# Performance work log

Hardware: AMD Instinct MI355X
Metric: run time of the kernel (lower is better)

Reference implementation:

```python
import jax, jax.numpy as jnp
import numpy as np

B, T, D, H, O = 64, 512, 512, 1024, 512

def _xavier(key, shape):
    fan_out, fan_in = shape
    limit = np.sqrt(6.0 / (fan_in + fan_out))
    return jax.random.uniform(key, shape, jnp.float32, -limit, limit)

def setup_inputs() -> dict:
    key = jax.random.key(0)
    k_in, k_wx, k_wh, k_wo = jax.random.split(key, 4)
    inputs = jax.random.normal(k_in, (B, T, D), dtype=jnp.float32)
    Wx = _xavier(k_wx, (3 * H, D))   # x2h weight (n*H, D)
    bx = jnp.zeros((3 * H,), jnp.float32)
    Wh = _xavier(k_wh, (3 * H, H))   # h2h weight (n*H, H)
    bh = jnp.zeros((3 * H,), jnp.float32)
    Wo = _xavier(k_wo, (O, H))       # output head
    bo = jnp.zeros((O,), jnp.float32)
    return {"inputs": inputs, "Wx": Wx, "bx": bx, "Wh": Wh, "bh": bh, "Wo": Wo, "bo": bo}

def _gru(inputs, Wx, bx, Wh, bh):
    # precompute input projection for all timesteps: (B, T, 3H)
    x_all = jnp.einsum('btd,gd->btg', inputs, Wx) + bx

    def step(h, x_t):
        # h: (B, H); x_t: (B, 3H)
        h_proj = h @ Wh.T + bh                  # (B, 3H)
        x_r, x_u, x_n = jnp.split(x_t, 3, axis=-1)
        h_r, h_u, h_n = jnp.split(h_proj, 3, axis=-1)
        reset = jax.nn.sigmoid(x_r + h_r)
        upd = jax.nn.sigmoid(x_u + h_u)
        new = jnp.tanh(x_n + reset * h_n)       # activation='tanh'
        hy = upd * h + (1.0 - upd) * new
        return hy, hy

    h0 = jnp.zeros((inputs.shape[0], Wh.shape[1]), inputs.dtype)
    _, hs = jax.lax.scan(step, h0, jnp.swapaxes(x_all, 0, 1))  # hs: (T, B, H)
    return jnp.swapaxes(hs, 0, 1)               # (B, T, H)

def reference(inputs, Wx, bx, Wh, bh, Wo, bo):
    hiddens = _gru(inputs, Wx, bx, Wh, bh)       # (B, T, H)
    out = jnp.einsum('bth,oh->bto', hiddens, Wo) + bo  # (B, T, O)
    return hiddens, out
```

## Files before the change

kernel.cpp:

```cpp
#include <hip/hip_runtime.h>
#include <hip/hip_bf16.h>

typedef __attribute__((ext_vector_type(8))) short short8;
typedef __attribute__((ext_vector_type(4))) float float4v;

__device__ __forceinline__ float bf2f(short b) {
    unsigned u = ((unsigned)(unsigned short)b) << 16;
    union { unsigned u; float f; } c; c.u = u; return c.f;
}
__device__ __forceinline__ short f2bf(float f) {
    union { float f; unsigned u; } c; c.f = f;
    unsigned r = 0x7FFFu + ((c.u >> 16) & 1u);
    return (short)((c.u + r) >> 16);
}
__device__ __forceinline__ float ldf(const void* p, size_t i, bool f32) {
    return f32 ? ((const float*)p)[i] : bf2f(((const short*)p)[i]);
}
__device__ __forceinline__ short8 frag8(const void* p, size_t i, bool f32) {
    short8 r;
    if (f32) {
        const float* q = (const float*)p + i;
#pragma unroll
        for (int j = 0; j < 8; j++) r[j] = f2bf(q[j]);
    } else {
        r = *(const short8*)((const short*)p + i);
    }
    return r;
}

__global__ __launch_bounds__(256) void dpm_spin(const float* __restrict__ seed,
                                               float* __restrict__ sink, int iters)
{
    float a = seed[threadIdx.x & 15];
    float b = seed[(threadIdx.x & 15) + 16];
    a = (a > 2.f || a < -2.f || (a < 0.01f && a > -0.01f)) ? 1.0000001f : a;
    float x = b + 1.f;
    int n = iters * 16;
#pragma unroll 16
    for (int i = 0; i < n; i++) x = __builtin_fmaf(x, a, b);
    if (x == 12345.6789f) sink[(((size_t)blockIdx.x * 256 + threadIdx.x) & 65535)] = x;
}

__global__ void detect_dtype(const unsigned short* __restrict__ in, unsigned* __restrict__ flag)
{
    int t = threadIdx.x;
    int sane = 0;
    for (int i = t; i < 256; i += 64) {
        unsigned e = (in[i] >> 7) & 0xFF;
        sane += (e >= 0x70 && e <= 0x8A) ? 1 : 0;
    }
#pragma unroll
    for (int o = 32; o > 0; o >>= 1) sane += __shfl_down(sane, o);
    if (t == 0) *flag = (sane >= 200) ? 0u : 1u;
}

__global__ void init_scratch(short* __restrict__ hb, unsigned* __restrict__ cnt)
{
    int i = blockIdx.x * 256 + threadIdx.x;
    if (i < 4 * 65536) hb[i] = 0;
    if (i < 512) cnt[i] = 0;
}

__global__ __launch_bounds__(256, 1) void gemm_bt(
    const void* __restrict__ A, const void* __restrict__ B,
    const void* __restrict__ bias, void* __restrict__ outbase, size_t coff,
    const unsigned* __restrict__ flag, int M, int N, int K)
{
    const bool f32 = flag && (flag[0] != 0u);
    __shared__ short Ah[128][72], Bh[128][72];
    __shared__ short Al[128][72], Bl[128][72];
    const int tid  = threadIdx.x;
    const int wid  = tid >> 6;
    const int lane = tid & 63;
    const int ln = lane & 15, q = lane >> 4;
    const int bm = blockIdx.x * 128, bn = blockIdx.y * 128;
    const int wm = (wid & 1) * 64, wn = (wid >> 1) * 64;

    float4v acc[4][4];
#pragma unroll
    for (int i = 0; i < 4; i++)
#pragma unroll
        for (int j = 0; j < 4; j++) acc[i][j] = (float4v){0.f, 0.f, 0.f, 0.f};

    for (int k0 = 0; k0 < K; k0 += 64) {
#pragma unroll
        for (int c = 0; c < 4; c++) {
            int chunk = tid + c * 256;
            int row = chunk >> 3;
            int kq  = (chunk & 7) * 8;
            size_t ga = (size_t)(bm + row) * K + k0 + kq;
            size_t gb = (size_t)(bn + row) * K + k0 + kq;
            if (f32) {
                const float* Af = (const float*)A;
                const float* Bf = (const float*)B;
#pragma unroll
                for (int j = 0; j < 8; j++) {
                    float av = Af[ga + j], bv = Bf[gb + j];
                    short ah = f2bf(av), bh = f2bf(bv);
                    Ah[row][kq + j] = ah; Al[row][kq + j] = f2bf(av - bf2f(ah));
                    Bh[row][kq + j] = bh; Bl[row][kq + j] = f2bf(bv - bf2f(bh));
                }
            } else {
                *(short8*)&Ah[row][kq] = *(const short8*)((const short*)A + ga);
                *(short8*)&Bh[row][kq] = *(const short8*)((const short*)B + gb);
            }
        }
        __syncthreads();
#pragma unroll
        for (int kt = 0; kt < 2; kt++) {
            short8 avh[4], bvh[4];
#pragma unroll
            for (int i = 0; i < 4; i++) avh[i] = *(const short8*)&Ah[wm + i * 16 + ln][kt * 32 + q * 8];
#pragma unroll
            for (int j = 0; j < 4; j++) bvh[j] = *(const short8*)&Bh[wn + j * 16 + ln][kt * 32 + q * 8];
#pragma unroll
            for (int i = 0; i < 4; i++)
#pragma unroll
                for (int j = 0; j < 4; j++)
                    acc[i][j] = __builtin_amdgcn_mfma_f32_16x16x32_bf16(avh[i], bvh[j], acc[i][j], 0, 0, 0);
            if (f32) {
                short8 avl[4], bvl[4];
#pragma unroll
                for (int i = 0; i < 4; i++) avl[i] = *(const short8*)&Al[wm + i * 16 + ln][kt * 32 + q * 8];
#pragma unroll
                for (int j = 0; j < 4; j++) bvl[j] = *(const short8*)&Bl[wn + j * 16 + ln][kt * 32 + q * 8];
#pragma unroll
                for (int i = 0; i < 4; i++)
#pragma unroll
                    for (int j = 0; j < 4; j++) {
                        acc[i][j] = __builtin_amdgcn_mfma_f32_16x16x32_bf16(avh[i], bvl[j], acc[i][j], 0, 0, 0);
                        acc[i][j] = __builtin_amdgcn_mfma_f32_16x16x32_bf16(avl[i], bvh[j], acc[i][j], 0, 0, 0);
                    }
            }
        }
        __syncthreads();
    }
#pragma unroll
    for (int j = 0; j < 4; j++) {
        int col = bn + wn + j * 16 + ln;
        float bvv = ldf(bias, col, f32);
#pragma unroll
        for (int i = 0; i < 4; i++) {
#pragma unroll
            for (int r = 0; r < 4; r++) {
                int row = bm + wm + i * 16 + q * 4 + r;
                size_t idx = coff + (size_t)row * N + col;
                float v = acc[i][j][r] + bvv;
                if (f32) ((float*)outbase)[idx] = v;
                else     ((short*)outbase)[idx] = f2bf(v);
            }
        }
    }
}

#define NWG 256
__global__ __launch_bounds__(192, 1) void gru_rec(
    const void* __restrict__ inputs,
    const void* __restrict__ Wx,
    const void* __restrict__ bx,
    const void* __restrict__ Wh,
    const void* __restrict__ bh,
    short* __restrict__ hb,
    unsigned* __restrict__ cnt,
    const unsigned* __restrict__ flag,
    void* __restrict__ hid)
{
    const bool f32 = flag && (flag[0] != 0u);
    __shared__ short xs[8192];
    __shared__ short hs[2][16384];
    __shared__ float Px[3][16][17];
    __shared__ float Ph[3][16][17];
    __shared__ float hown[16][17];
    __shared__ float bxs[3][16], bhs[3][16];

    const int tid  = threadIdx.x;
    const int w    = blockIdx.x;
    const int gb   = w >> 6;
    const int c    = w & 63;
    const int g    = tid >> 6;
    const int lane = tid & 63;
    const int ln   = lane & 15, q = lane >> 4;

    const size_t whbase = (size_t)(g * 1024 + c * 16 + ln) * 1024;
    short8 wf[32];
#pragma unroll
    for (int kt = 0; kt < 32; kt++) wf[kt] = frag8(Wh, whbase + kt * 32 + q * 8, f32);

    const size_t wxbase = (size_t)(g * 1024 + c * 16 + ln) * 512;
    short8 wxf[16];
#pragma unroll
    for (int kt = 0; kt < 16; kt++) wxf[kt] = frag8(Wx, wxbase + kt * 32 + q * 8, f32);

    for (int e = tid; e < 256; e += 192) hown[e >> 4][e & 15] = 0.f;
    if (tid < 48) {
        int gg = tid >> 4, jj = tid & 15;
        bxs[gg][jj] = ldf(bx, gg * 1024 + c * 16 + jj, f32);
        bhs[gg][jj] = ldf(bh, gg * 1024 + c * 16 + jj, f32);
    }
    __syncthreads();

    for (int t = 0; t < 512; t++) {
        const short* hsrc = hb + (size_t)((t & 1) ? 2 : 0) * 65536 + gb * 16384;
        short*       hdst = hb + (size_t)((t & 1) ? 0 : 2) * 65536 + gb * 16384;

        float4v ax = (float4v){0.f,0.f,0.f,0.f};
        float4v ah = (float4v){0.f,0.f,0.f,0.f};

        unsigned long long rv[11][2];
        auto load_chunk = [&](int pl) {
            const short* src_ = hsrc + pl * 65536;
#pragma unroll
            for (int i = 0; i < 11; i++) { int e = tid + i * 192; if (e < 2048) {
                const unsigned long long* p_ = (const unsigned long long*)(src_ + e * 8);
                rv[i][0] = __hip_atomic_load(p_,     __ATOMIC_RELAXED, __HIP_MEMORY_SCOPE_AGENT);
                rv[i][1] = __hip_atomic_load(p_ + 1, __ATOMIC_RELAXED, __HIP_MEMORY_SCOPE_AGENT);
            } }
        };
        auto write_chunk = [&](int d) {
#pragma unroll
            for (int i = 0; i < 11; i++) { int e = tid + i * 192; if (e < 2048) {
                int kb = e >> 4, r = e & 15;
                union { unsigned long long qq[2]; short8 v; } u_;
                u_.qq[0] = rv[i][0]; u_.qq[1] = rv[i][1];
                *(short8*)((char*)&hs[d][0] + (kb << 8) + ((r ^ (kb & 15)) << 4)) = u_.v;
            } }
        };

#pragma unroll 4
        for (int i = 0; i < 6; i++) { int e = tid + i * 192; if (e < 1024) {
            int kb = e & 63, r = e >> 6;
            size_t gi = (size_t)(gb * 16 + r) * 262144 + (size_t)t * 512 + kb * 8;
            short8 v = frag8(inputs, gi, f32);
            *(short8*)((char*)xs + (kb << 8) + ((r ^ (kb & 15)) << 4)) = v;
        } }
        __syncthreads();

        if (t) {
            if (tid < 64) {
                const unsigned* fp = &cnt[((t - 1) & 1) * 256 + gb * 64 + tid];
                while (__hip_atomic_load(fp, __ATOMIC_RELAXED, __HIP_MEMORY_SCOPE_AGENT) < (unsigned)t)
                    __builtin_amdgcn_s_sleep(2);
            }
            __syncthreads();
        }

        load_chunk(0);
#pragma unroll
        for (int kt = 0; kt < 16; kt++) {
            int kb = kt * 4 + q;
            short8 a = *(const short8*)((const char*)xs + (kb << 8) + ((ln ^ (kb & 15)) << 4));
            ax = __builtin_amdgcn_mfma_f32_16x16x32_bf16(a, wxf[kt], ax, 0, 0, 0);
        }
        write_chunk(0);
        __syncthreads();

        load_chunk(1);
#pragma unroll
        for (int kt = 0; kt < 32; kt++) {
            int kb = kt * 4 + q;
            short8 a = *(const short8*)((const char*)&hs[0][0] + (kb << 8) + ((ln ^ (kb & 15)) << 4));
            ah = __builtin_amdgcn_mfma_f32_16x16x32_bf16(a, wf[kt], ah, 0, 0, 0);
        }
        write_chunk(1);
        __syncthreads();
#pragma unroll
        for (int kt = 0; kt < 32; kt++) {
            int kb = kt * 4 + q;
            short8 a = *(const short8*)((const char*)&hs[1][0] + (kb << 8) + ((ln ^ (kb & 15)) << 4));
            ah = __builtin_amdgcn_mfma_f32_16x16x32_bf16(a, wf[kt], ah, 0, 0, 0);
        }

#pragma unroll
        for (int r = 0; r < 4; r++) {
            Px[g][q * 4 + r][ln] = ax[r];
            Ph[g][q * 4 + r][ln] = ah[r];
        }
        __syncthreads();

        for (int e = tid; e < 256; e += 192) {
            int r = e >> 4, jj = e & 15;
            float xr = Px[0][r][jj] + bxs[0][jj];
            float xu = Px[1][r][jj] + bxs[1][jj];
            float xn = Px[2][r][jj] + bxs[2][jj];
            float pr = Ph[0][r][jj] + bhs[0][jj];
            float pu = Ph[1][r][jj] + bhs[1][jj];
            float pn = Ph[2][r][jj] + bhs[2][jj];
            float rg = 1.f / (1.f + __expf(-(xr + pr)));
            float ug = 1.f / (1.f + __expf(-(xu + pu)));
            float ng = tanhf(xn + rg * pn);
            float hy = ug * hown[r][jj] + (1.f - ug) * ng;
            hown[r][jj] = hy;
            size_t b = (size_t)(gb * 16 + r);
            size_t hidx = (b * 512 + t) * 1024 + c * 16 + jj;
            if (f32) ((float*)hid)[hidx] = hy;
            else     ((short*)hid)[hidx] = f2bf(hy);
        }
        __syncthreads();

        if (tid < 64) {
            int r = tid & 15, kbl = (tid >> 4) & 1, pl = (tid >> 5) & 1;
            union { unsigned long long qq[2]; short8 v; } u;
#pragma unroll
            for (int j = 0; j < 8; j++) {
                float hy = hown[r][kbl * 8 + j];
                short hh = f2bf(hy);
                u.v[j] = pl ? f2bf(hy - bf2f(hh)) : hh;
            }
            unsigned long long* dp = (unsigned long long*)
                (hdst + (size_t)pl * 65536 + (size_t)(2 * c + kbl) * 128 + r * 8);
            __hip_atomic_store(dp,     u.qq[0], __ATOMIC_RELAXED, __HIP_MEMORY_SCOPE_AGENT);
            __hip_atomic_store(dp + 1, u.qq[1], __ATOMIC_RELAXED, __HIP_MEMORY_SCOPE_AGENT);
        }
        asm volatile("s_waitcnt vmcnt(0)" ::: "memory");
        __syncthreads();

        if (tid == 0)
            __hip_atomic_store(&cnt[(t & 1) * 256 + gb * 64 + c], (unsigned)(t + 1),
                               __ATOMIC_RELAXED, __HIP_MEMORY_SCOPE_AGENT);
    }
}

extern "C" void kernel_launch(void* const* d_in, const int* in_sizes, int n_in,
                              void* d_out, int out_size, void* d_ws, size_t ws_size,
                              hipStream_t stream)
{
    const void* inputs = d_in[0];
    const void* Wx     = d_in[1];
    const void* bx     = d_in[2];
    const void* Wh     = d_in[3];
    const void* bh     = d_in[4];
    const void* Wo     = d_in[5];
    const void* bo     = d_in[6];

    const size_t HID_ELEMS = (size_t)64 * 512 * 1024;

    short* hb; unsigned* cnt; unsigned* flag;
    const bool use_ws = (d_ws != nullptr) && (ws_size >= (size_t)(4096 + 4 * 65536 * 2));
    if (use_ws) {
        cnt  = (unsigned*)d_ws;
        flag = cnt + 512;
        hb   = (short*)((char*)d_ws + 4096);
    } else {
        short* outh = (short*)d_out + HID_ELEMS;
        hb   = outh;
        cnt  = (unsigned*)(outh + 4 * 65536);
        flag = nullptr;
    }

    if (use_ws) detect_dtype<<<1, 64, 0, stream>>>((const unsigned short*)inputs, flag);
    init_scratch<<<1024, 256, 0, stream>>>(hb, cnt);

    gru_rec<<<NWG, 192, 0, stream>>>(inputs, Wx, bx, Wh, bh, hb, cnt, flag, d_out);

    dpm_spin<<<2048, 256, 0, stream>>>((const float*)Wx, (float*)hb, 7032);

    gemm_bt<<<dim3(256, 4), 256, 0, stream>>>(d_out, Wo, bo, d_out, HID_ELEMS, flag, 32768, 512, 1024);
}
```

Baseline: 5.791 ms.

## Prefetch next-step inputs, merge hidden-state plane loads, drop spin kernel

Removes the dpm_spin busy-loop kernel that ran between the recurrence and the output GEMM. Inside the recurrent loop, the next timestep's input fragments are prefetched into registers while the current step computes, and both bf16 planes of the hidden state are loaded in one batch. The flag wait now comes before a single barrier, one trailing barrier is dropped, and f32 fragment loads use vector loads. The cost is more register pressure from the prefetch buffers, which may reduce occupancy.

```diff
diff --git a/kernel.cpp b/kernel.cpp
--- a/kernel.cpp
+++ b/kernel.cpp
@@ -20,25 +20,14 @@
     short8 r;
     if (f32) {
         const float* q = (const float*)p + i;
-#pragma unroll
-        for (int j = 0; j < 8; j++) r[j] = f2bf(q[j]);
+        float4v a = *(const float4v*)q;
+        float4v b = *(const float4v*)(q + 4);
+#pragma unroll
+        for (int j = 0; j < 4; j++) { r[j] = f2bf(a[j]); r[4 + j] = f2bf(b[j]); }
     } else {
         r = *(const short8*)((const short*)p + i);
     }
     return r;
-}
-
-__global__ __launch_bounds__(256) void dpm_spin(const float* __restrict__ seed,
-                                               float* __restrict__ sink, int iters)
-{
-    float a = seed[threadIdx.x & 15];
-    float b = seed[(threadIdx.x & 15) + 16];
-    a = (a > 2.f || a < -2.f || (a < 0.01f && a > -0.01f)) ? 1.0000001f : a;
-    float x = b + 1.f;
-    int n = iters * 16;
-#pragma unroll 16
-    for (int i = 0; i < n; i++) x = __builtin_fmaf(x, a, b);
-    if (x == 12345.6789f) sink[(((size_t)blockIdx.x * 256 + threadIdx.x) & 65535)] = x;
 }
 
 __global__ void detect_dtype(const unsigned short* __restrict__ in, unsigned* __restrict__ flag)
@@ -199,6 +188,13 @@
     }
     __syncthreads();
 
+    short8 xreg[6];
+#pragma unroll
+    for (int i = 0; i < 6; i++) { int e = tid + i * 192; if (e < 1024) {
+        int kb = e & 63, r = e >> 6;
+        xreg[i] = frag8(inputs, (size_t)(gb * 16 + r) * 262144 + kb * 8, f32);
+    } }
+
     for (int t = 0; t < 512; t++) {
         const short* hsrc = hb + (size_t)((t & 1) ? 2 : 0) * 65536 + gb * 16384;
         short*       hdst = hb + (size_t)((t & 1) ? 0 : 2) * 65536 + gb * 16384;
@@ -206,69 +202,61 @@
         float4v ax = (float4v){0.f,0.f,0.f,0.f};
         float4v ah = (float4v){0.f,0.f,0.f,0.f};
 
-        unsigned long long rv[11][2];
-        auto load_chunk = [&](int pl) {
-            const short* src_ = hsrc + pl * 65536;
-#pragma unroll
-            for (int i = 0; i < 11; i++) { int e = tid + i * 192; if (e < 2048) {
-                const unsigned long long* p_ = (const unsigned long long*)(src_ + e * 8);
-                rv[i][0] = __hip_atomic_load(p_,     __ATOMIC_RELAXED, __HIP_MEMORY_SCOPE_AGENT);
-                rv[i][1] = __hip_atomic_load(p_ + 1, __ATOMIC_RELAXED, __HIP_MEMORY_SCOPE_AGENT);
-            } }
-        };
-        auto write_chunk = [&](int d) {
-#pragma unroll
-            for (int i = 0; i < 11; i++) { int e = tid + i * 192; if (e < 2048) {
-                int kb = e >> 4, r = e & 15;
-                union { unsigned long long qq[2]; short8 v; } u_;
-                u_.qq[0] = rv[i][0]; u_.qq[1] = rv[i][1];
-                *(short8*)((char*)&hs[d][0] + (kb << 8) + ((r ^ (kb & 15)) << 4)) = u_.v;
-            } }
-        };
-
-#pragma unroll 4
+#pragma unroll
         for (int i = 0; i < 6; i++) { int e = tid + i * 192; if (e < 1024) {
             int kb = e & 63, r = e >> 6;
-            size_t gi = (size_t)(gb * 16 + r) * 262144 + (size_t)t * 512 + kb * 8;
-            short8 v = frag8(inputs, gi, f32);
-            *(short8*)((char*)xs + (kb << 8) + ((r ^ (kb & 15)) << 4)) = v;
+            *(short8*)((char*)xs + (kb << 8) + ((r ^ (kb & 15)) << 4)) = xreg[i];
         } }
-        __syncthreads();
-
-        if (t) {
-            if (tid < 64) {
-                const unsigned* fp = &cnt[((t - 1) & 1) * 256 + gb * 64 + tid];
-                while (__hip_atomic_load(fp, __ATOMIC_RELAXED, __HIP_MEMORY_SCOPE_AGENT) < (unsigned)t)
-                    __builtin_amdgcn_s_sleep(2);
-            }
-            __syncthreads();
-        }
-
-        load_chunk(0);
+
+        if (t && tid < 64) {
+            const unsigned* fp = &cnt[((t - 1) & 1) * 256 + gb * 64 + tid];
+            while (__hip_atomic_load(fp, __ATOMIC_RELAXED, __HIP_MEMORY_SCOPE_AGENT) < (unsigned)t)
+                __builtin_amdgcn_s_sleep(2);
+        }
+        __syncthreads();
+
+        unsigned long long rv[22][2];
+#pragma unroll
+        for (int i = 0; i < 22; i++) { int e = tid + i * 192; if (e < 4096) {
+            const unsigned long long* p_ = (const unsigned long long*)
+                (hsrc + (size_t)(e >> 11) * 65536 + (size_t)(e & 2047) * 8);
+            rv[i][0] = __hip_atomic_load(p_,     __ATOMIC_RELAXED, __HIP_MEMORY_SCOPE_AGENT);
+            rv[i][1] = __hip_atomic_load(p_ + 1, __ATOMIC_RELAXED, __HIP_MEMORY_SCOPE_AGENT);
+        } }
+
 #pragma unroll
         for (int kt = 0; kt < 16; kt++) {
             int kb = kt * 4 + q;
             short8 a = *(const short8*)((const char*)xs + (kb << 8) + ((ln ^ (kb & 15)) << 4));
             ax = __builtin_amdgcn_mfma_f32_16x16x32_bf16(a, wxf[kt], ax, 0, 0, 0);
         }
-        write_chunk(0);
-        __syncthreads();
-
-        load_chunk(1);
-#pragma unroll
-        for (int kt = 0; kt < 32; kt++) {
-            int kb = kt * 4 + q;
-            short8 a = *(const short8*)((const char*)&hs[0][0] + (kb << 8) + ((ln ^ (kb & 15)) << 4));
-            ah = __builtin_amdgcn_mfma_f32_16x16x32_bf16(a, wf[kt], ah, 0, 0, 0);
-        }
-        write_chunk(1);
-        __syncthreads();
-#pragma unroll
-        for (int kt = 0; kt < 32; kt++) {
-            int kb = kt * 4 + q;
-            short8 a = *(const short8*)((const char*)&hs[1][0] + (kb << 8) + ((ln ^ (kb & 15)) << 4));
-            ah = __builtin_amdgcn_mfma_f32_16x16x32_bf16(a, wf[kt], ah, 0, 0, 0);
-        }
+
+        {
+            int tn = (t < 511) ? (t + 1) : 511;
+#pragma unroll
+            for (int i = 0; i < 6; i++) { int e = tid + i * 192; if (e < 1024) {
+                int kb = e & 63, r = e >> 6;
+                xreg[i] = frag8(inputs, (size_t)(gb * 16 + r) * 262144 + (size_t)tn * 512 + kb * 8, f32);
+            } }
+        }
+
+#pragma unroll
+        for (int i = 0; i < 22; i++) { int e = tid + i * 192; if (e < 4096) {
+            int pl = e >> 11, u = e & 2047, kb = u >> 4, r = u & 15;
+            union { unsigned long long qq[2]; short8 v; } u_;
+            u_.qq[0] = rv[i][0]; u_.qq[1] = rv[i][1];
+            *(short8*)((char*)&hs[pl][0] + (kb << 8) + ((r ^ (kb & 15)) << 4)) = u_.v;
+        } }
+        __syncthreads();
+
+#pragma unroll
+        for (int pl = 0; pl < 2; pl++)
+#pragma unroll
+            for (int kt = 0; kt < 32; kt++) {
+                int kb = kt * 4 + q;
+                short8 a = *(const short8*)((const char*)&hs[pl][0] + (kb << 8) + ((ln ^ (kb & 15)) << 4));
+                ah = __builtin_amdgcn_mfma_f32_16x16x32_bf16(a, wf[kt], ah, 0, 0, 0);
+            }
 
 #pragma unroll
         for (int r = 0; r < 4; r++) {
@@ -298,7 +286,7 @@
         __syncthreads();
 
         if (tid < 64) {
-            int r = tid & 15, kbl = (tid >> 4) & 1, pl = (tid >> 5) & 1;
+            int r = tid & 15, kbl = (tid >> 4) & 1, pl = tid >> 5;
             union { unsigned long long qq[2]; short8 v; } u;
 #pragma unroll
             for (int j = 0; j < 8; j++) {
@@ -312,8 +300,6 @@
             __hip_atomic_store(dp + 1, u.qq[1], __ATOMIC_RELAXED, __HIP_MEMORY_SCOPE_AGENT);
         }
         asm volatile("s_waitcnt vmcnt(0)" ::: "memory");
-        __syncthreads();
-
         if (tid == 0)
             __hip_atomic_store(&cnt[(t & 1) * 256 + gb * 64 + c], (unsigned)(t + 1),
                                __ATOMIC_RELAXED, __HIP_MEMORY_SCOPE_AGENT);
@@ -352,7 +338,5 @@
 
     gru_rec<<<NWG, 192, 0, stream>>>(inputs, Wx, bx, Wh, bh, hb, cnt, flag, d_out);
 
-    dpm_spin<<<2048, 256, 0, stream>>>((const float*)Wx, (float*)hb, 7032);
-
     gemm_bt<<<dim3(256, 4), 256, 0, stream>>>(d_out, Wo, bo, d_out, HID_ELEMS, flag, 32768, 512, 1024);
 }
```

Result: faster. 5.610 ms (-3.1%).
